# Kernel optimization log

Hardware: AMD Instinct MI355X
Metric: run time of the kernel (lower is better)

The kernel has to match this reference:

```python
import jax, jax.numpy as jnp
import numpy as np

TAU = 2.0          # LIF membrane time constant (init kwarg)
ALPHA = 2.0        # spikingjelly surrogate.ATan default alpha
V_TH = 1.0         # spikingjelly LIFNode default v_threshold

# Heaviside spike with ATan surrogate gradient (spikingjelly semantics)
@jax.custom_vjp
def spike(v):
    return (v >= V_TH).astype(v.dtype)

def _spike_fwd(v):
    return spike(v), v

def _spike_bwd(v, g):
    sg = (ALPHA / 2.0) / (1.0 + (jnp.pi / 2.0 * ALPHA * (v - V_TH)) ** 2)
    return (g * sg,)

spike.defvjp(_spike_fwd, _spike_bwd)

def lif(x):
    # Fresh LIFNode: v_prev = 0, v_reset = 0, decay_input=True
    # charge: v = v_prev + (x - (v_prev - v_reset)) / tau  ->  v = x / tau
    return spike(x / TAU)

def setup_inputs() -> dict:
    key = jax.random.key(0)
    ks = jax.random.split(key, 5)
    B = 2097152
    # kaiming-uniform-ish scale: 1/sqrt(fan_in)
    def w(k, out_f, in_f):
        return jax.random.normal(k, (out_f, in_f), dtype=jnp.float32) / np.sqrt(in_f)
    return {
        "x": jax.random.normal(ks[0], (B, 5), dtype=jnp.float32),
        "W1": w(ks[1], 32, 5),
        "W2": w(ks[2], 32, 32),
        "W3": w(ks[3], 16, 32),
        "W4": w(ks[4], 10, 16),
    }

def reference(x, W1, W2, W3, W4):
    # fc: Linear(5,32)->LIF -> Linear(32,32)->LIF -> Linear(32,16)->LIF
    s = lif(x @ W1.T)          # [B, 32]
    s = lif(s @ W2.T)          # [B, 32]
    s = lif(s @ W3.T)          # [B, 16]
    # fc1: Linear(16,10)->LIF
    return lif(s @ W4.T)       # [B, 10]
```

## Files before the change

kernel.cpp:

```cpp
#include <hip/hip_runtime.h>


typedef float v4f __attribute__((ext_vector_type(4)));
typedef float v2f __attribute__((ext_vector_type(2)));

#define TPB 256
#define RPL 4
#define WROWS (64 * RPL)
#define RPB (TPB * RPL)

__global__ __launch_bounds__(64) void snn_prep(
    const float* __restrict__ W1,
    const float* __restrict__ W2,
    float* __restrict__ ws)
{
    const int t = threadIdx.x;
    float mm = -3.4e38f;
    if (t < 32) {
#pragma unroll
        for (int k = 0; k < 5; ++k) ws[k * 32 + t] = W1[t * 5 + k];
        mm = W2[t];
#pragma unroll
        for (int j = 1; j < 32; ++j) mm = fmaxf(mm, W2[j * 32 + t]);
        ws[160 + t] = mm;
    }
#pragma unroll
    for (int off = 32; off; off >>= 1) mm = fmaxf(mm, __shfl_xor(mm, off));
    if (t == 0) ws[192] = mm;
}

__global__ __launch_bounds__(TPB) void snn_fused(
    const float* __restrict__ x,
    const float* __restrict__ W2,
    const float* __restrict__ W3,
    const float* __restrict__ W4,
    const float* __restrict__ ws,
    float* __restrict__ out,
    int B)
{
    __shared__ __align__(16) float stage[4][WROWS * 10];

    const int t = threadIdx.x;
    const int wv = t >> 6, lane = t & 63;
    float* sbuf = stage[wv];
    const long wrow0 = (long)blockIdx.x * RPB + (long)wv * WROWS;
    if (wrow0 >= B) return;

    const v2f* __restrict__ w1p = (const v2f*)ws;
    const float* __restrict__ smx = ws + 160;
    const float mxmax = ws[192];

    if (wrow0 + WROWS <= B) {
        const v4f* xg = (const v4f*)(x + wrow0 * 5);
        v4f* s4 = (v4f*)sbuf;
#pragma unroll
        for (int e = 0; e < 5; ++e) s4[e * 64 + lane] = xg[e * 64 + lane];

        v4f xq[5];
        {
            const v4f* sx = (const v4f*)(sbuf + lane * 20);
#pragma unroll
            for (int e = 0; e < 5; ++e) xq[e] = sx[e];
        }
        const float* xf = (const float*)xq;

        {
            v4f z = {0.0f, 0.0f, 0.0f, 0.0f};
#pragma unroll
            for (int e = 0; e < 10; ++e) s4[e * 64 + lane] = z;
        }

        unsigned m[RPL] = {0u, 0u, 0u, 0u};
#pragma unroll
        for (int j2 = 0; j2 < 16; ++j2) {
            const v2f wa = w1p[j2], wb = w1p[16 + j2], wc = w1p[32 + j2];
            const v2f wd = w1p[48 + j2], we = w1p[64 + j2];
#pragma unroll
            for (int c = 0; c < RPL; ++c) {
                v2f h = xf[c * 5 + 0] * wa;
                h += xf[c * 5 + 1] * wb;
                h += xf[c * 5 + 2] * wc;
                h += xf[c * 5 + 3] * wd;
                h += xf[c * 5 + 4] * we;
                if (h.x >= 2.0f) m[c] |= (1u << (2 * j2));
                if (h.y >= 2.0f) m[c] |= (1u << (2 * j2 + 1));
            }
        }

#pragma unroll
        for (int c = 0; c < RPL; ++c) {
            const unsigned mc = m[c];
            if (mc && ((float)__popc(mc) * mxmax >= 1.998f)) {
                float S = 0.0f;
                unsigned mm = mc;
                while (mm) { int i = __ffs(mm) - 1; mm &= mm - 1; S += smx[i]; }
                if (S >= 1.998f) {
                    float h2[32];
#pragma unroll
                    for (int j = 0; j < 32; ++j) h2[j] = 0.0f;
                    mm = mc;
                    while (mm) {
                        const int i = __ffs(mm) - 1;
                        mm &= mm - 1;
                        const float* col = W2 + i;
#pragma unroll
                        for (int j = 0; j < 32; ++j) h2[j] += col[j * 32];
                    }
                    unsigned m2 = 0u;
#pragma unroll
                    for (int j = 0; j < 32; ++j)
                        if (h2[j] >= 2.0f) m2 |= (1u << j);

                    if (m2) {
                        unsigned m3 = 0u;
#pragma unroll
                        for (int j = 0; j < 16; ++j) {
                            float g = 0.0f;
#pragma unroll
                            for (int i = 0; i < 32; ++i)
                                if ((m2 >> i) & 1u) g += W3[j * 32 + i];
                            if (g >= 2.0f) m3 |= (1u << j);
                        }
                        float* orow = sbuf + (lane * RPL + c) * 10;
#pragma unroll
                        for (int j = 0; j < 10; ++j) {
                            float g = 0.0f;
#pragma unroll
                            for (int i = 0; i < 16; ++i)
                                if ((m3 >> i) & 1u) g += W4[j * 16 + i];
                            orow[j] = (g >= 2.0f) ? 1.0f : 0.0f;
                        }
                    }
                }
            }
        }

        v4f* og = (v4f*)(out + wrow0 * 10);
        const v4f* s4c = (const v4f*)sbuf;
#pragma unroll
        for (int e = 0; e < 10; ++e)
            __builtin_nontemporal_store(s4c[e * 64 + lane], &og[e * 64 + lane]);
    } else {
        for (int c = 0; c < RPL; ++c) {
            const long r = wrow0 + (long)lane * RPL + c;
            if (r >= B) continue;
            float xr[5];
#pragma unroll
            for (int k = 0; k < 5; ++k) xr[k] = x[r * 5 + k];
            unsigned mc = 0u;
#pragma unroll
            for (int j2 = 0; j2 < 16; ++j2) {
                v2f h = xr[0] * w1p[j2];
                h += xr[1] * w1p[16 + j2];
                h += xr[2] * w1p[32 + j2];
                h += xr[3] * w1p[48 + j2];
                h += xr[4] * w1p[64 + j2];
                if (h.x >= 2.0f) mc |= (1u << (2 * j2));
                if (h.y >= 2.0f) mc |= (1u << (2 * j2 + 1));
            }
            float o[10];
#pragma unroll
            for (int j = 0; j < 10; ++j) o[j] = 0.0f;
            if (mc && ((float)__popc(mc) * mxmax >= 1.998f)) {
                float S = 0.0f;
                unsigned mm = mc;
                while (mm) { int i = __ffs(mm) - 1; mm &= mm - 1; S += smx[i]; }
                if (S >= 1.998f) {
                    float h2[32];
#pragma unroll
                    for (int j = 0; j < 32; ++j) h2[j] = 0.0f;
                    mm = mc;
                    while (mm) {
                        const int i = __ffs(mm) - 1;
                        mm &= mm - 1;
                        const float* col = W2 + i;
#pragma unroll
                        for (int j = 0; j < 32; ++j) h2[j] += col[j * 32];
                    }
                    unsigned m2 = 0u;
#pragma unroll
                    for (int j = 0; j < 32; ++j)
                        if (h2[j] >= 2.0f) m2 |= (1u << j);
                    if (m2) {
                        unsigned m3 = 0u;
#pragma unroll
                        for (int j = 0; j < 16; ++j) {
                            float g = 0.0f;
#pragma unroll
                            for (int i = 0; i < 32; ++i)
                                if ((m2 >> i) & 1u) g += W3[j * 32 + i];
                            if (g >= 2.0f) m3 |= (1u << j);
                        }
#pragma unroll
                        for (int j = 0; j < 10; ++j) {
                            float g = 0.0f;
#pragma unroll
                            for (int i = 0; i < 16; ++i)
                                if ((m3 >> i) & 1u) g += W4[j * 16 + i];
                            o[j] = (g >= 2.0f) ? 1.0f : 0.0f;
                        }
                    }
                }
            }
#pragma unroll
            for (int j = 0; j < 10; ++j) out[r * 10 + j] = o[j];
        }
    }
}

extern "C" void kernel_launch(void* const* d_in, const int* in_sizes, int n_in,
                              void* d_out, int out_size, void* d_ws, size_t ws_size,
                              hipStream_t stream) {
    const float* x  = (const float*)d_in[0];
    const float* W1 = (const float*)d_in[1];
    const float* W2 = (const float*)d_in[2];
    const float* W3 = (const float*)d_in[3];
    const float* W4 = (const float*)d_in[4];
    float* out = (float*)d_out;
    float* ws  = (float*)d_ws;

    int B = in_sizes[0] / 5;
    snn_prep<<<1, 64, 0, stream>>>(W1, W2, ws);
    int grid = (B + RPB - 1) / RPB;
    snn_fused<<<grid, TPB, 0, stream>>>(x, W2, W3, W4, ws, out, B);
}
```

Before: 158.0 us.

## Halve rows per lane and add wave-wide all-zero fast path for output stores

Reduces rows per lane from four to two, doubling grid size and lowering per-thread register and shared-memory footprint. It also splits layer-2 classification from layers 3-4 and, when no row in the wavefront yields any layer-2 spike, writes zeros directly to global memory, skipping the shared-memory zeroing and staging round trip. The fast path saves LDS traffic for the common all-zero case. Halving the work per wave doubles the number of wavefronts and repeats the per-wave setup.

```diff
diff --git a/kernel.cpp b/kernel.cpp
--- a/kernel.cpp
+++ b/kernel.cpp
@@ -5,7 +5,7 @@
 typedef float v2f __attribute__((ext_vector_type(2)));
 
 #define TPB 256
-#define RPL 4
+#define RPL 2
 #define WROWS (64 * RPL)
 #define RPB (TPB * RPL)
 
@@ -54,23 +54,20 @@
         const v4f* xg = (const v4f*)(x + wrow0 * 5);
         v4f* s4 = (v4f*)sbuf;
 #pragma unroll
-        for (int e = 0; e < 5; ++e) s4[e * 64 + lane] = xg[e * 64 + lane];
-
-        v4f xq[5];
+        for (int e = 0; e < 3; ++e) {
+            int idx = e * 64 + lane;
+            if (idx < (WROWS * 5) / 4) s4[idx] = xg[idx];
+        }
+
+        v2f xp[5];
         {
-            const v4f* sx = (const v4f*)(sbuf + lane * 20);
-#pragma unroll
-            for (int e = 0; e < 5; ++e) xq[e] = sx[e];
-        }
-        const float* xf = (const float*)xq;
-
-        {
-            v4f z = {0.0f, 0.0f, 0.0f, 0.0f};
-#pragma unroll
-            for (int e = 0; e < 10; ++e) s4[e * 64 + lane] = z;
-        }
-
-        unsigned m[RPL] = {0u, 0u, 0u, 0u};
+            const v2f* sx = (const v2f*)(sbuf + lane * 10);
+#pragma unroll
+            for (int e = 0; e < 5; ++e) xp[e] = sx[e];
+        }
+        const float* xf = (const float*)xp;
+
+        unsigned m[RPL] = {0u, 0u};
 #pragma unroll
         for (int j2 = 0; j2 < 16; ++j2) {
             const v2f wa = w1p[j2], wb = w1p[16 + j2], wc = w1p[32 + j2];
@@ -87,8 +84,13 @@
             }
         }
 
+        bool dense[RPL];
+        unsigned m2s[RPL];
+        bool any_dense = false;
 #pragma unroll
         for (int c = 0; c < RPL; ++c) {
+            dense[c] = false;
+            m2s[c] = 0u;
             const unsigned mc = m[c];
             if (mc && ((float)__popc(mc) * mxmax >= 1.998f)) {
                 float S = 0.0f;
@@ -110,36 +112,53 @@
 #pragma unroll
                     for (int j = 0; j < 32; ++j)
                         if (h2[j] >= 2.0f) m2 |= (1u << j);
-
-                    if (m2) {
-                        unsigned m3 = 0u;
-#pragma unroll
-                        for (int j = 0; j < 16; ++j) {
-                            float g = 0.0f;
-#pragma unroll
-                            for (int i = 0; i < 32; ++i)
-                                if ((m2 >> i) & 1u) g += W3[j * 32 + i];
-                            if (g >= 2.0f) m3 |= (1u << j);
-                        }
-                        float* orow = sbuf + (lane * RPL + c) * 10;
-#pragma unroll
-                        for (int j = 0; j < 10; ++j) {
-                            float g = 0.0f;
-#pragma unroll
-                            for (int i = 0; i < 16; ++i)
-                                if ((m3 >> i) & 1u) g += W4[j * 16 + i];
-                            orow[j] = (g >= 2.0f) ? 1.0f : 0.0f;
-                        }
-                    }
-                }
-            }
-        }
-
-        v4f* og = (v4f*)(out + wrow0 * 10);
-        const v4f* s4c = (const v4f*)sbuf;
-#pragma unroll
-        for (int e = 0; e < 10; ++e)
-            __builtin_nontemporal_store(s4c[e * 64 + lane], &og[e * 64 + lane]);
+                    m2s[c] = m2;
+                    if (m2) { dense[c] = true; any_dense = true; }
+                }
+            }
+        }
+
+        if (!__any(any_dense)) {
+            v4f z = {0.0f, 0.0f, 0.0f, 0.0f};
+            v4f* og = (v4f*)(out + wrow0 * 10);
+#pragma unroll
+            for (int e = 0; e < 5; ++e)
+                __builtin_nontemporal_store(z, &og[e * 64 + lane]);
+        } else {
+            {
+                v4f z = {0.0f, 0.0f, 0.0f, 0.0f};
+#pragma unroll
+                for (int e = 0; e < 5; ++e) s4[e * 64 + lane] = z;
+            }
+#pragma unroll
+            for (int c = 0; c < RPL; ++c) {
+                if (!dense[c]) continue;
+                const unsigned m2 = m2s[c];
+                unsigned m3 = 0u;
+#pragma unroll
+                for (int j = 0; j < 16; ++j) {
+                    float g = 0.0f;
+#pragma unroll
+                    for (int i = 0; i < 32; ++i)
+                        if ((m2 >> i) & 1u) g += W3[j * 32 + i];
+                    if (g >= 2.0f) m3 |= (1u << j);
+                }
+                float* orow = sbuf + (lane * RPL + c) * 10;
+#pragma unroll
+                for (int j = 0; j < 10; ++j) {
+                    float g = 0.0f;
+#pragma unroll
+                    for (int i = 0; i < 16; ++i)
+                        if ((m3 >> i) & 1u) g += W4[j * 16 + i];
+                    orow[j] = (g >= 2.0f) ? 1.0f : 0.0f;
+                }
+            }
+            v4f* og = (v4f*)(out + wrow0 * 10);
+            const v4f* s4c = (const v4f*)sbuf;
+#pragma unroll
+            for (int e = 0; e < 5; ++e)
+                __builtin_nontemporal_store(s4c[e * 64 + lane], &og[e * 64 + lane]);
+        }
     } else {
         for (int c = 0; c < RPL; ++c) {
             const long r = wrow0 + (long)lane * RPL + c;
```

Measured after the change: 166.5 us. 5.4% more time.
